# Kernel tuning notes

Hardware: AMD Instinct MI355X
Metric: run time of the kernel (lower is better)

Reference implementation:

```python
import jax, jax.numpy as jnp
import numpy as np

N_NODES = 100000
N_EDGES = 1600000
D_IN = 256
D_OUT = 64


def setup_inputs() -> dict:
    key = jax.random.key(0)
    k1, k2, k3, k4, k5 = jax.random.split(key, 5)
    features = jax.random.normal(k1, (N_NODES, D_IN), dtype=jnp.float32)
    # Xavier-uniform style init for the weight
    limit = float(np.sqrt(6.0 / (D_IN + D_OUT)))
    weight = jax.random.uniform(k2, (D_IN, D_OUT), minval=-limit, maxval=limit, dtype=jnp.float32)
    adj_rows = jax.random.randint(k3, (N_EDGES,), 0, N_NODES, dtype=jnp.int64)
    adj_cols = jax.random.randint(k4, (N_EDGES,), 0, N_NODES, dtype=jnp.int64)
    adj_values = jax.random.uniform(k5, (N_EDGES,), dtype=jnp.float32)
    return {"features": features, "weight": weight, "adj_rows": adj_rows,
            "adj_cols": adj_cols, "adj_values": adj_values}


def reference(features, weight, adj_rows, adj_cols, adj_values):
    # support = features @ W  -> [N, D_OUT]
    support = jnp.matmul(features, weight)
    # spmm: out[r] = sum_e (v_e * support[c_e]) for edges (r, c, v)
    msgs = adj_values[:, None] * support[adj_cols]  # [E, D_OUT]
    output = jax.ops.segment_sum(msgs, adj_rows, num_segments=features.shape[0])
    # active=True -> ReLU fused on the aggregation output
    return jax.nn.relu(output)
```

## Files before the change

### kernel.cpp

```cpp
#include <hip/hip_runtime.h>

#define N_NODES 100000
#define N_EDGES 1600000
#define D_IN    256
#define D_OUT   64

#define BROWS 256
#define NBUCK ((N_NODES + BROWS - 1) / BROWS)
#define CAP   8192
#define EB    8192
#define NB1   ((N_EDGES + EB - 1) / EB)
#define MAXB  8192

typedef __attribute__((ext_vector_type(8))) short short8_t;
typedef __attribute__((ext_vector_type(4))) float f32x4;

static __device__ __forceinline__ unsigned short f2bf(float f) {
    unsigned u = __builtin_bit_cast(unsigned, f);
    unsigned r = u + 0x7FFFu + ((u >> 16) & 1u);
    return (unsigned short)(r >> 16);
}
static __device__ __forceinline__ float bf2f(unsigned short h) {
    return __builtin_bit_cast(float, (unsigned)h << 16);
}
static __device__ __forceinline__ unsigned cvt_pk_bf16(float lo, float hi) {
    unsigned r;
    asm("v_cvt_pk_bf16_f32 %0, %1, %2" : "=v"(r) : "v"(lo), "v"(hi));
    return r;
}

__global__ __launch_bounds__(256) void gemm_kernel(const float* __restrict__ feat,
                                                   const float* __restrict__ W,
                                                   unsigned short* __restrict__ support,
                                                   int* __restrict__ gcursor) {
    __shared__ unsigned short Wf[2048 * 8];
    const int tid = threadIdx.x;

    if (blockIdx.x == 0) {
        for (int i = tid; i < NBUCK; i += 256) gcursor[i] = i * CAP;
    }

    #pragma unroll
    for (int i = 0; i < 8; ++i) {
        const int slot = i * 256 + tid;
        const int s  = slot >> 8;
        const int nt = (slot >> 6) & 3;
        const int l  = slot & 63;
        const int kbase = s * 32 + ((l >> 4) * 8);
        const int col   = nt * 16 + (l & 15);
        unsigned short tmp[8];
        #pragma unroll
        for (int e = 0; e < 8; ++e)
            tmp[e] = f2bf(W[(size_t)(kbase + e) * D_OUT + col]);
        *(short8_t*)&Wf[slot * 8] = *(short8_t*)tmp;
    }
    __syncthreads();

    const int lane = tid & 63;
    const int wave = tid >> 6;
    const int row0 = blockIdx.x * 64 + wave * 16;
    if (row0 >= N_NODES) return;

    const float* arow = feat + (size_t)(row0 + (lane & 15)) * D_IN + ((lane >> 4) * 8);

    f32x4 acc[4];
    #pragma unroll
    for (int nt = 0; nt < 4; ++nt) acc[nt] = (f32x4){0.f, 0.f, 0.f, 0.f};

    #pragma unroll
    for (int s = 0; s < 8; ++s) {
        const float4 a0 = *(const float4*)(arow + s * 32);
        const float4 a1 = *(const float4*)(arow + s * 32 + 4);
        unsigned u[4];
        u[0] = cvt_pk_bf16(a0.x, a0.y);
        u[1] = cvt_pk_bf16(a0.z, a0.w);
        u[2] = cvt_pk_bf16(a1.x, a1.y);
        u[3] = cvt_pk_bf16(a1.z, a1.w);
        const short8_t av = *(short8_t*)u;
        #pragma unroll
        for (int nt = 0; nt < 4; ++nt) {
            const short8_t bv = *(short8_t*)&Wf[((s * 4 + nt) * 64 + lane) * 8];
            acc[nt] = __builtin_amdgcn_mfma_f32_16x16x32_bf16(av, bv, acc[nt], 0, 0, 0);
        }
    }

    #pragma unroll
    for (int nt = 0; nt < 4; ++nt) {
        #pragma unroll
        for (int reg = 0; reg < 4; ++reg) {
            const int row = row0 + (lane >> 4) * 4 + reg;
            const int col = nt * 16 + (lane & 15);
            support[(size_t)row * D_OUT + col] = f2bf(acc[nt][reg]);
        }
    }
}

__global__ __launch_bounds__(1024) void bscatter_kernel(const int*   __restrict__ rows,
                                                        const int*   __restrict__ cols,
                                                        const float* __restrict__ vals,
                                                        int*  __restrict__ gcursor,
                                                        int2* __restrict__ pack) {
    __shared__ int lrows[EB];
    __shared__ int h[NBUCK];
    __shared__ int base[NBUCK];
    const int tid = threadIdx.x;
    for (int i = tid; i < NBUCK; i += 1024) h[i] = 0;
    __syncthreads();

    const int e0 = blockIdx.x * EB;
    for (int i = tid; i < EB; i += 1024) {
        const int e = e0 + i;
        const int r = (e < N_EDGES) ? rows[e] : -1;
        lrows[i] = r;
        if (r >= 0) atomicAdd(&h[r >> 8], 1);
    }
    __syncthreads();

    for (int b = tid; b < NBUCK; b += 1024) {
        const int c = h[b];
        base[b] = c ? atomicAdd(&gcursor[b], c) : 0;
        h[b] = 0;
    }
    __syncthreads();

    for (int i = tid; i < EB; i += 1024) {
        const int r = lrows[i];
        if (r < 0) continue;
        const int b = r >> 8;
        const int pos = base[b] + atomicAdd(&h[b], 1);
        if (pos < (b + 1) * CAP) {
            const int e = e0 + i;
            pack[pos] = make_int2(((r & 255) << 17) | cols[e], __float_as_int(vals[e]));
        }
    }
}

__global__ __launch_bounds__(1024) void breduce_kernel(const int*  __restrict__ gcursor,
                                                       const int2* __restrict__ pack,
                                                       const unsigned short* __restrict__ support,
                                                       float* __restrict__ out) {
    __shared__ int2 ps[MAXB];
    __shared__ int cnt[BROWS];
    __shared__ int ofs[BROWS];
    __shared__ int cur[BROWS];
    __shared__ int scn[BROWS];
    const int b     = blockIdx.x;
    const int tid   = threadIdx.x;
    const int start = b * CAP;
    int n = gcursor[b] - start;
    if (n > MAXB) n = MAXB;
    const int lane  = tid & 63;
    const int wave  = tid >> 6;
    const int half  = lane >> 5;
    const int cl    = lane & 31;

    if (tid < BROWS) cnt[tid] = 0;
    __syncthreads();

    for (int i = tid; i < n; i += 1024)
        atomicAdd(&cnt[pack[start + i].x >> 17], 1);
    __syncthreads();

    const int v = (tid < BROWS) ? cnt[tid] : 0;
    if (tid < BROWS) scn[tid] = v;
    __syncthreads();
    #pragma unroll
    for (int off = 1; off < BROWS; off <<= 1) {
        const int t = (tid < BROWS && tid >= off) ? scn[tid - off] : 0;
        __syncthreads();
        if (tid < BROWS) scn[tid] += t;
        __syncthreads();
    }
    if (tid < BROWS) { ofs[tid] = scn[tid] - v; cur[tid] = 0; }
    __syncthreads();

    for (int i = tid; i < n; i += 1024) {
        const int2 p  = pack[start + i];
        const int  rl = p.x >> 17;
        ps[ofs[rl] + atomicAdd(&cur[rl], 1)] = p;
    }
    __syncthreads();

    for (int rl = wave; rl < BROWS; rl += 16) {
        const int row = b * BROWS + rl;
        if (row >= N_NODES) continue;
        const int s0 = ofs[rl];
        const int nr = cnt[rl];
        float ax0 = 0.f, ay0 = 0.f, ax1 = 0.f, ay1 = 0.f;
        float ax2 = 0.f, ay2 = 0.f, ax3 = 0.f, ay3 = 0.f;
        int k = 0;
        for (; k + 7 < nr; k += 8) {
            const int2 p0 = ps[s0 + k     + half];
            const int2 p1 = ps[s0 + k + 2 + half];
            const int2 p2 = ps[s0 + k + 4 + half];
            const int2 p3 = ps[s0 + k + 6 + half];
            const unsigned q0 = *(const unsigned*)&support[(size_t)(p0.x & 0x1FFFF) * D_OUT + 2 * cl];
            const unsigned q1 = *(const unsigned*)&support[(size_t)(p1.x & 0x1FFFF) * D_OUT + 2 * cl];
            const unsigned q2 = *(const unsigned*)&support[(size_t)(p2.x & 0x1FFFF) * D_OUT + 2 * cl];
            const unsigned q3 = *(const unsigned*)&support[(size_t)(p3.x & 0x1FFFF) * D_OUT + 2 * cl];
            const float v0 = __int_as_float(p0.y);
            const float v1 = __int_as_float(p1.y);
            const float v2 = __int_as_float(p2.y);
            const float v3 = __int_as_float(p3.y);
            ax0 = fmaf(v0, bf2f((unsigned short)(q0 & 0xFFFF)), ax0);
            ay0 = fmaf(v0, bf2f((unsigned short)(q0 >> 16)),    ay0);
            ax1 = fmaf(v1, bf2f((unsigned short)(q1 & 0xFFFF)), ax1);
            ay1 = fmaf(v1, bf2f((unsigned short)(q1 >> 16)),    ay1);
            ax2 = fmaf(v2, bf2f((unsigned short)(q2 & 0xFFFF)), ax2);
            ay2 = fmaf(v2, bf2f((unsigned short)(q2 >> 16)),    ay2);
            ax3 = fmaf(v3, bf2f((unsigned short)(q3 & 0xFFFF)), ax3);
            ay3 = fmaf(v3, bf2f((unsigned short)(q3 >> 16)),    ay3);
        }
        for (; k + 1 < nr; k += 2) {
            const int2 p = ps[s0 + k + half];
            const unsigned q = *(const unsigned*)&support[(size_t)(p.x & 0x1FFFF) * D_OUT + 2 * cl];
            const float vv = __int_as_float(p.y);
            ax0 = fmaf(vv, bf2f((unsigned short)(q & 0xFFFF)), ax0);
            ay0 = fmaf(vv, bf2f((unsigned short)(q >> 16)),    ay0);
        }
        if (k < nr && half == 0) {
            const int2 p = ps[s0 + k];
            const unsigned q = *(const unsigned*)&support[(size_t)(p.x & 0x1FFFF) * D_OUT + 2 * cl];
            const float vv = __int_as_float(p.y);
            ax0 = fmaf(vv, bf2f((unsigned short)(q & 0xFFFF)), ax0);
            ay0 = fmaf(vv, bf2f((unsigned short)(q >> 16)),    ay0);
        }
        float sx = (ax0 + ax1) + (ax2 + ax3);
        float sy = (ay0 + ay1) + (ay2 + ay3);
        sx += __shfl_xor(sx, 32, 64);
        sy += __shfl_xor(sy, 32, 64);
        if (half == 0) {
            float2 o;
            o.x = fmaxf(sx, 0.f);
            o.y = fmaxf(sy, 0.f);
            *(float2*)&out[(size_t)row * D_OUT + 2 * cl] = o;
        }
    }
}

extern "C" void kernel_launch(void* const* d_in, const int* in_sizes, int n_in,
                              void* d_out, int out_size, void* d_ws, size_t ws_size,
                              hipStream_t stream) {
    const float* feat = (const float*)d_in[0];
    const float* W    = (const float*)d_in[1];
    const int*   rows = (const int*)d_in[2];
    const int*   cols = (const int*)d_in[3];
    const float* vals = (const float*)d_in[4];
    float*       out  = (float*)d_out;

    unsigned short* support = (unsigned short*)d_ws;
    int*   gcursor = (int*)(support + 6400000);
    int2*  pack    = (int2*)(gcursor + 392);

    gemm_kernel<<<(N_NODES + 63) / 64, 256, 0, stream>>>(feat, W, support, gcursor);

    bscatter_kernel<<<NB1, 1024, 0, stream>>>(rows, cols, vals, gcursor, pack);

    breduce_kernel<<<NBUCK, 1024, 0, stream>>>(gcursor, pack, support, out);
}
```

Before: 85.88 us.

## Merge GEMM and edge bucket-scatter into one heterogeneous launch

The GEMM and the edge bucketing scatter, which are independent, now run in one kernel whose blocks branch by block index, so both phases can occupy the GPU at the same time. Cursor initialisation moves to a small separate kernel. Block size drops to 512 and GEMM blocks now cover 128 rows each. This trades one extra tiny launch and a shared-memory footprint sized for the larger scatter path against overlapping a memory-bound scatter with the compute-and-bandwidth GEMM.

```diff
diff --git a/kernel.cpp b/kernel.cpp
--- a/kernel.cpp
+++ b/kernel.cpp
@@ -9,7 +9,8 @@
 #define NBUCK ((N_NODES + BROWS - 1) / BROWS)
 #define CAP   8192
 #define EB    8192
-#define NB1   ((N_EDGES + EB - 1) / EB)
+#define NSB   ((N_EDGES + EB - 1) / EB)
+#define NGB   ((N_NODES + 127) / 128)
 #define MAXB  8192
 
 typedef __attribute__((ext_vector_type(8))) short short8_t;
@@ -29,108 +30,111 @@
     return r;
 }
 
-__global__ __launch_bounds__(256) void gemm_kernel(const float* __restrict__ feat,
-                                                   const float* __restrict__ W,
-                                                   unsigned short* __restrict__ support,
-                                                   int* __restrict__ gcursor) {
-    __shared__ unsigned short Wf[2048 * 8];
-    const int tid = threadIdx.x;
-
-    if (blockIdx.x == 0) {
-        for (int i = tid; i < NBUCK; i += 256) gcursor[i] = i * CAP;
-    }
-
-    #pragma unroll
-    for (int i = 0; i < 8; ++i) {
-        const int slot = i * 256 + tid;
-        const int s  = slot >> 8;
-        const int nt = (slot >> 6) & 3;
-        const int l  = slot & 63;
-        const int kbase = s * 32 + ((l >> 4) * 8);
-        const int col   = nt * 16 + (l & 15);
-        unsigned short tmp[8];
-        #pragma unroll
-        for (int e = 0; e < 8; ++e)
-            tmp[e] = f2bf(W[(size_t)(kbase + e) * D_OUT + col]);
-        *(short8_t*)&Wf[slot * 8] = *(short8_t*)tmp;
-    }
-    __syncthreads();
-
-    const int lane = tid & 63;
-    const int wave = tid >> 6;
-    const int row0 = blockIdx.x * 64 + wave * 16;
-    if (row0 >= N_NODES) return;
-
-    const float* arow = feat + (size_t)(row0 + (lane & 15)) * D_IN + ((lane >> 4) * 8);
-
-    f32x4 acc[4];
-    #pragma unroll
-    for (int nt = 0; nt < 4; ++nt) acc[nt] = (f32x4){0.f, 0.f, 0.f, 0.f};
-
-    #pragma unroll
-    for (int s = 0; s < 8; ++s) {
-        const float4 a0 = *(const float4*)(arow + s * 32);
-        const float4 a1 = *(const float4*)(arow + s * 32 + 4);
-        unsigned u[4];
-        u[0] = cvt_pk_bf16(a0.x, a0.y);
-        u[1] = cvt_pk_bf16(a0.z, a0.w);
-        u[2] = cvt_pk_bf16(a1.x, a1.y);
-        u[3] = cvt_pk_bf16(a1.z, a1.w);
-        const short8_t av = *(short8_t*)u;
-        #pragma unroll
-        for (int nt = 0; nt < 4; ++nt) {
-            const short8_t bv = *(short8_t*)&Wf[((s * 4 + nt) * 64 + lane) * 8];
-            acc[nt] = __builtin_amdgcn_mfma_f32_16x16x32_bf16(av, bv, acc[nt], 0, 0, 0);
-        }
-    }
-
-    #pragma unroll
-    for (int nt = 0; nt < 4; ++nt) {
-        #pragma unroll
-        for (int reg = 0; reg < 4; ++reg) {
-            const int row = row0 + (lane >> 4) * 4 + reg;
-            const int col = nt * 16 + (lane & 15);
-            support[(size_t)row * D_OUT + col] = f2bf(acc[nt][reg]);
-        }
-    }
-}
-
-__global__ __launch_bounds__(1024) void bscatter_kernel(const int*   __restrict__ rows,
+__global__ __launch_bounds__(512) void init_kernel(int* __restrict__ gcursor) {
+    const int i = threadIdx.x;
+    if (i < NBUCK) gcursor[i] = i * CAP;
+}
+
+__global__ __launch_bounds__(512, 8) void phase1_kernel(const float* __restrict__ feat,
+                                                        const float* __restrict__ W,
+                                                        const int*   __restrict__ rows,
                                                         const int*   __restrict__ cols,
                                                         const float* __restrict__ vals,
+                                                        unsigned short* __restrict__ support,
                                                         int*  __restrict__ gcursor,
                                                         int2* __restrict__ pack) {
-    __shared__ int lrows[EB];
-    __shared__ int h[NBUCK];
-    __shared__ int base[NBUCK];
+    __shared__ int smem[EB + 2 * NBUCK];
     const int tid = threadIdx.x;
-    for (int i = tid; i < NBUCK; i += 1024) h[i] = 0;
-    __syncthreads();
-
-    const int e0 = blockIdx.x * EB;
-    for (int i = tid; i < EB; i += 1024) {
-        const int e = e0 + i;
-        const int r = (e < N_EDGES) ? rows[e] : -1;
-        lrows[i] = r;
-        if (r >= 0) atomicAdd(&h[r >> 8], 1);
-    }
-    __syncthreads();
-
-    for (int b = tid; b < NBUCK; b += 1024) {
-        const int c = h[b];
-        base[b] = c ? atomicAdd(&gcursor[b], c) : 0;
-        h[b] = 0;
-    }
-    __syncthreads();
-
-    for (int i = tid; i < EB; i += 1024) {
-        const int r = lrows[i];
-        if (r < 0) continue;
-        const int b = r >> 8;
-        const int pos = base[b] + atomicAdd(&h[b], 1);
-        if (pos < (b + 1) * CAP) {
+
+    if (blockIdx.x < NSB) {
+        int* lrows = smem;
+        int* h     = smem + EB;
+        int* base  = h + NBUCK;
+        for (int i = tid; i < NBUCK; i += 512) h[i] = 0;
+        __syncthreads();
+
+        const int e0 = blockIdx.x * EB;
+        for (int i = tid; i < EB; i += 512) {
             const int e = e0 + i;
-            pack[pos] = make_int2(((r & 255) << 17) | cols[e], __float_as_int(vals[e]));
+            const int r = (e < N_EDGES) ? rows[e] : -1;
+            lrows[i] = r;
+            if (r >= 0) atomicAdd(&h[r >> 8], 1);
+        }
+        __syncthreads();
+
+        for (int b = tid; b < NBUCK; b += 512) {
+            const int c = h[b];
+            base[b] = c ? atomicAdd(&gcursor[b], c) : 0;
+            h[b] = 0;
+        }
+        __syncthreads();
+
+        for (int i = tid; i < EB; i += 512) {
+            const int r = lrows[i];
+            if (r < 0) continue;
+            const int b = r >> 8;
+            const int pos = base[b] + atomicAdd(&h[b], 1);
+            if (pos < (b + 1) * CAP) {
+                const int e = e0 + i;
+                pack[pos] = make_int2(((r & 255) << 17) | cols[e], __float_as_int(vals[e]));
+            }
+        }
+    } else {
+        const int gb = blockIdx.x - NSB;
+        unsigned short* Wf = (unsigned short*)smem;
+
+        #pragma unroll
+        for (int i = 0; i < 4; ++i) {
+            const int slot = i * 512 + tid;
+            const int s  = slot >> 8;
+            const int nt = (slot >> 6) & 3;
+            const int l  = slot & 63;
+            const int kbase = s * 32 + ((l >> 4) * 8);
+            const int col   = nt * 16 + (l & 15);
+            unsigned short tmp[8];
+            #pragma unroll
+            for (int e = 0; e < 8; ++e)
+                tmp[e] = f2bf(W[(size_t)(kbase + e) * D_OUT + col]);
+            *(short8_t*)&Wf[slot * 8] = *(short8_t*)tmp;
+        }
+        __syncthreads();
+
+        const int lane = tid & 63;
+        const int wave = tid >> 6;
+        const int row0 = gb * 128 + wave * 16;
+        if (row0 >= N_NODES) return;
+
+        const float* arow = feat + (size_t)(row0 + (lane & 15)) * D_IN + ((lane >> 4) * 8);
+
+        f32x4 acc[4];
+        #pragma unroll
+        for (int nt = 0; nt < 4; ++nt) acc[nt] = (f32x4){0.f, 0.f, 0.f, 0.f};
+
+        #pragma unroll
+        for (int s = 0; s < 8; ++s) {
+            const float4 a0 = *(const float4*)(arow + s * 32);
+            const float4 a1 = *(const float4*)(arow + s * 32 + 4);
+            unsigned u[4];
+            u[0] = cvt_pk_bf16(a0.x, a0.y);
+            u[1] = cvt_pk_bf16(a0.z, a0.w);
+            u[2] = cvt_pk_bf16(a1.x, a1.y);
+            u[3] = cvt_pk_bf16(a1.z, a1.w);
+            const short8_t av = *(short8_t*)u;
+            #pragma unroll
+            for (int nt = 0; nt < 4; ++nt) {
+                const short8_t bv = *(short8_t*)&Wf[((s * 4 + nt) * 64 + lane) * 8];
+                acc[nt] = __builtin_amdgcn_mfma_f32_16x16x32_bf16(av, bv, acc[nt], 0, 0, 0);
+            }
+        }
+
+        #pragma unroll
+        for (int nt = 0; nt < 4; ++nt) {
+            #pragma unroll
+            for (int reg = 0; reg < 4; ++reg) {
+                const int row = row0 + (lane >> 4) * 4 + reg;
+                const int col = nt * 16 + (lane & 15);
+                support[(size_t)row * D_OUT + col] = f2bf(acc[nt][reg]);
+            }
         }
     }
 }
@@ -252,9 +256,10 @@
     int*   gcursor = (int*)(support + 6400000);
     int2*  pack    = (int2*)(gcursor + 392);
 
-    gemm_kernel<<<(N_NODES + 63) / 64, 256, 0, stream>>>(feat, W, support, gcursor);
-
-    bscatter_kernel<<<NB1, 1024, 0, stream>>>(rows, cols, vals, gcursor, pack);
+    init_kernel<<<1, 512, 0, stream>>>(gcursor);
+
+    phase1_kernel<<<NSB + NGB, 512, 0, stream>>>(feat, W, rows, cols, vals,
+                                                 support, gcursor, pack);
 
     breduce_kernel<<<NBUCK, 1024, 0, stream>>>(gcursor, pack, support, out);
 }
```

New measurement: 81.53 us. 1.05x faster.
